# Performance work log

Measured on AMD Instinct MI355X. Metric: run time of the kernel, lower is better.

The kernel has to match this reference:

```python
import jax, jax.numpy as jnp
import numpy as np

# Fixed architecture constants (match init_kwargs)
B, CIN, H, W = 2, 3, 224, 224
COUT = 64
KH = KW = 7
SH = SW = 2
PAD = 3
GROUPS = 1
MIX = 4
CG = COUT // GROUPS          # channels per group
REL = CG // 2                # rel_size
PH, PW = H + 2 * PAD, W + 2 * PAD          # padded spatial dims (230, 230)
FH = (PH - KH) // SH + 1                    # output height (112)
FW = (PW - KW) // SW + 1                    # output width  (112)


def setup_inputs() -> dict:
    key = jax.random.key(0)
    ks = jax.random.split(key, 10)
    n = jax.random.normal
    return {
        "x": n(ks[0], (B, CIN, H, W), jnp.float32),
        "weight_query": n(ks[1], (GROUPS, CIN // GROUPS, CG), jnp.float32) * 0.2,
        "weight_key": n(ks[2], (GROUPS, CIN // GROUPS, CG), jnp.float32) * 0.2,
        "weight_value": n(ks[3], (MIX, GROUPS, CIN // GROUPS, CG), jnp.float32) * 0.2,
        "relative_x": n(ks[4], (REL, 1, KW), jnp.float32) * 0.1,
        "relative_y": n(ks[5], (CG - REL, KH, 1), jnp.float32) * 0.1,
        "emb_x": n(ks[6], (CG, 1, PW), jnp.float32) * 0.1,
        "emb_y": n(ks[7], (CG, PH, 1), jnp.float32) * 0.1,
        "emb_m": n(ks[8], (MIX, CG, 1, 1), jnp.float32) * 0.1,
        "bias": n(ks[9], (COUT,), jnp.float32) * 0.05,
    }


def _unfold(t):
    """torch.nn.functional.unfold: (b,c,PH,PW) -> (b,c,KH*KW,FH*FW) with (c,kh,kw) layout."""
    b, c = t.shape[0], t.shape[1]
    ri = jnp.arange(FH) * SH
    rj = jnp.arange(FW) * SW
    p = t[:, :, ri[:, None] + jnp.arange(KH)[None, :], :]          # (b,c,FH,KH,PW)
    p = p[:, :, :, :, rj[:, None] + jnp.arange(KW)[None, :]]       # (b,c,FH,KH,FW,KW)
    return p.transpose(0, 1, 3, 5, 2, 4).reshape(b, c, KH * KW, FH * FW)


def _forward(x, wq, wk, wv, rx, ry, ex, ey, em, bias):
    b = x.shape[0]
    # relative position bias: (COUT, KH*KW, 1)
    rel = jnp.concatenate([jnp.tile(rx, (1, KH, 1)), jnp.tile(ry, (1, 1, KW))], axis=0)
    rel = jnp.tile(rel, (GROUPS, 1, 1)).reshape(COUT, KH * KW, 1)

    xp = jnp.pad(x, ((0, 0), (0, 0), (PAD, PAD), (PAD, PAD)))       # (b,CIN,PH,PW)
    x_ij = xp.transpose(0, 2, 3, 1).reshape(b, PH * PW, GROUPS, CIN // GROUPS)

    # per-pixel grouped projections -> (b, COUT, PH, PW)
    vq = jnp.einsum('bngi,gio->bgon', x_ij, wq).reshape(b, COUT, PH, PW)
    vk = jnp.einsum('bngi,gio->bgon', x_ij, wk).reshape(b, COUT, PH, PW)

    # mixture weights over value transforms: softmax over mix axis, per pixel
    p_ab = ex + ey                                                   # (CG,PH,PW)
    p_abm = jax.nn.softmax(jnp.sum(p_ab[None] * em, axis=1), axis=0) # (MIX,PH,PW)

    vvm = jnp.einsum('bngi,mgio->mbgon', x_ij, wv).reshape(MIX, b, COUT, PH, PW)
    vv = jnp.sum(vvm * p_abm[:, None, None], axis=0)                 # (b,COUT,PH,PW)

    win_k = _unfold(vk)                                              # (b,COUT,KH*KW,L)
    win_v = _unfold(vv)                                              # (b,COUT,KH*KW,L)
    # center query of each window (equivalent to unfold then slice center)
    ci = (KH - 1) // 2 + jnp.arange(FH) * SH
    cj = (KW - 1) // 2 + jnp.arange(FW) * SW
    win_q = vq[:, :, ci[:, None], cj[None, :]].reshape(b, COUT, 1, FH * FW)

    scores = jnp.sum(win_q * (win_k + rel[None]), axis=1)            # (b,KH*KW,L)
    # NOTE: the torch code applies softmax over dim=2 which, after the sum over
    # channels, is the SPATIAL dim (L), not the window dim. Faithful to source.
    attn = jax.nn.softmax(scores, axis=2)                            # (b,KH*KW,L)
    v = jnp.sum(attn[:, None] * win_v, axis=2) + bias[None, :, None] # (b,COUT,L)
    return v.reshape(b, COUT, FH, FW)


def reference(x, weight_query, weight_key, weight_value, relative_x, relative_y, emb_x, emb_y, emb_m, bias):
    return _forward(x, weight_query, weight_key, weight_value, relative_x, relative_y, emb_x, emb_y, emb_m, bias)
```

## Files before the change

kernel.cpp:

```cpp
#include <hip/hip_runtime.h>
#include <math.h>

namespace {
constexpr int Bc = 2, Hc = 224, Wc = 224, HWc = Hc * Wc;
constexpr int COUTc = 64, KHc = 7, KWc = 7, PADc = 3;
constexpr int MIXc = 4, RELc = 32;
constexpr int PHc = 230, PWc = 230;
constexpr int FHc = 112, FWc = 112, NN = FHc * FWc;
constexpr int NK = KHc * KWc;
constexpr int NCHUNK = 196;
constexpr int WS_EEX = 0;
constexpr int WS_EEY = WS_EEX + MIXc * PWc;
constexpr int WS_COL = WS_EEY + MIXc * PHc;
constexpr int WS_PART = 1920;
}

__global__ __launch_bounds__(256) void sam_k0(
    const float* __restrict__ ex, const float* __restrict__ ey,
    const float* __restrict__ em, const float* __restrict__ wq,
    const float* __restrict__ wk, const float* __restrict__ rx,
    const float* __restrict__ ry, float* __restrict__ ws) {
  const int idx = blockIdx.x * 256 + threadIdx.x;
  constexpr int half = MIXc * PWc;
  if (idx < 2 * half) {
    const int which = idx >= half;
    const int r = which ? idx - half : idx;
    const int m = r / PWc, j = r % PWc;
    float s = 0.f;
#pragma unroll 8
    for (int c = 0; c < COUTc; ++c)
      s += (which ? ey[c * PHc + j] : ex[c * PWc + j]) * em[m * COUTc + c];
    ws[idx] = __expf(s);
  }
  const int u = idx - 2 * half;
  if (u >= 0 && u < 51) {
    float s = 0.f;
    if (u < 9) {
      const int cj = u / 3, ci = u % 3;
#pragma unroll 8
      for (int o = 0; o < COUTc; ++o) s += wq[cj * COUTc + o] * wk[ci * COUTc + o];
    } else if (u < 30) {
      const int v = u - 9, cj = v / 7, kw = v % 7;
#pragma unroll 8
      for (int o = 0; o < RELc; ++o) s += wq[cj * COUTc + o] * rx[o * KWc + kw];
    } else {
      const int v = u - 30, cj = v / 7, kh = v % 7;
#pragma unroll 8
      for (int o = 0; o < RELc; ++o) s += wq[cj * COUTc + RELc + o] * ry[o * KHc + kh];
    }
    ws[WS_COL + u] = s;
  }
}

__global__ __launch_bounds__(256) void sam_stats(const float* __restrict__ x,
                                                 float* __restrict__ ws) {
  __shared__ float sCol[51];
  const int t = threadIdx.x;
  if (t < 51) sCol[t] = ws[WS_COL + t];
  __syncthreads();

  const int w = t >> 6, lane = t & 63;
  const int k = blockIdx.y * 4 + w;
  if (k >= NK) return;
  const int b = blockIdx.z;
  const int kh = k / 7, kw = k - 7 * kh;
  const int n = blockIdx.x * 64 + lane;
  const int fh = n / FWc, fw = n - fh * FWc;
  const int i0 = 2 * fh, j0 = 2 * fw;
  const float* xb = x + (size_t)b * 3 * HWc;
  const int co = i0 * Wc + j0;
  const float xc0 = xb[co], xc1 = xb[HWc + co], xc2 = xb[2 * HWc + co];

  float s = xc0 * (sCol[9 + kw] + sCol[30 + kh]) +
            xc1 * (sCol[16 + kw] + sCol[37 + kh]) +
            xc2 * (sCol[23 + kw] + sCol[44 + kh]);
  const int ir = i0 + kh - PADc, jc = j0 + kw - PADc;
  if ((unsigned)ir < (unsigned)Hc && (unsigned)jc < (unsigned)Wc) {
    const float q0 = xc0 * sCol[0] + xc1 * sCol[3] + xc2 * sCol[6];
    const float q1 = xc0 * sCol[1] + xc1 * sCol[4] + xc2 * sCol[7];
    const float q2 = xc0 * sCol[2] + xc1 * sCol[5] + xc2 * sCol[8];
    const int off = ir * Wc + jc;
    s += q0 * xb[off] + q1 * xb[HWc + off] + q2 * xb[2 * HWc + off];
  }
  float e = __expf(s);
#pragma unroll
  for (int m2 = 32; m2; m2 >>= 1) e += __shfl_xor(e, m2, 64);
  if (lane == 0)
    ws[WS_PART + ((size_t)b * NK + k) * NCHUNK + blockIdx.x] = e;
}

__global__ __launch_bounds__(256) void sam_out(
    const float* __restrict__ x, const float* __restrict__ wv,
    const float* __restrict__ bias, const float* __restrict__ ws,
    float* __restrict__ out) {
  __shared__ float sCol[51];
  __shared__ float sdninv[NK];
  __shared__ float swv[12 * 64];
  __shared__ float sbias[64];
  __shared__ float sT[8][32][13];

  const int t = threadIdx.x;
  const int b = blockIdx.y;
  if (t < 51) sCol[t] = ws[WS_COL + t];
  if (t < 64) sbias[t] = bias[t];
  for (int i = t; i < 12 * 64; i += 256) swv[i] = wv[i];
  if (t < 4 * NK) {
    const int k = t >> 2, p = t & 3;
    const float* base = ws + WS_PART + ((size_t)b * NK + k) * NCHUNK;
    float s = 0.f;
    for (int c = p; c < NCHUNK; c += 4) s += base[c];
    s += __shfl_xor(s, 1, 64);
    s += __shfl_xor(s, 2, 64);
    if (p == 0) sdninv[k] = 1.f / s;
  }
  __syncthreads();

  const int g = t >> 5, px = t & 31;
  const int n = blockIdx.x * 32 + px;
  const int fh = n / FWc, fw = n - fh * FWc;
  const int i0 = 2 * fh, j0 = 2 * fw;
  const float* xb = x + (size_t)b * 3 * HWc;
  const int co = i0 * Wc + j0;
  const float xc0 = xb[co], xc1 = xb[HWc + co], xc2 = xb[2 * HWc + co];
  const float q0 = xc0 * sCol[0] + xc1 * sCol[3] + xc2 * sCol[6];
  const float q1 = xc0 * sCol[1] + xc1 * sCol[4] + xc2 * sCol[7];
  const float q2 = xc0 * sCol[2] + xc1 * sCol[5] + xc2 * sCol[8];

  const float* eEX = ws + WS_EEX;
  const float* eEY = ws + WS_EEY;

  float T[12] = {0.f};
#pragma unroll
  for (int it = 0; it < 7; ++it) {
    const int kk = g + 8 * it;
    if (kk < NK) {
      const int kh = kk / 7, kw = kk - 7 * ((kk * 9363) >> 16);
      const int kw2 = kk - 7 * kh;
      (void)kw;
      const int ir = i0 + kh - PADc, jc = j0 + kw2 - PADc;
      if ((unsigned)ir < (unsigned)Hc && (unsigned)jc < (unsigned)Wc) {
        float s = xc0 * (sCol[9 + kw2] + sCol[30 + kh]) +
                  xc1 * (sCol[16 + kw2] + sCol[37 + kh]) +
                  xc2 * (sCol[23 + kw2] + sCol[44 + kh]);
        const int off = ir * Wc + jc;
        const float x0 = xb[off], x1 = xb[HWc + off], x2 = xb[2 * HWc + off];
        s += q0 * x0 + q1 * x1 + q2 * x2;
        const float e = __expf(s) * sdninv[kk];
        const int ii = i0 + kh, jj = j0 + kw2;
        const float p0 = eEX[jj] * eEY[ii];
        const float p1 = eEX[PWc + jj] * eEY[PHc + ii];
        const float p2 = eEX[2 * PWc + jj] * eEY[2 * PHc + ii];
        const float p3 = eEX[3 * PWc + jj] * eEY[3 * PHc + ii];
        const float wgt = e * __builtin_amdgcn_rcpf(p0 + p1 + p2 + p3);
        const float a0 = wgt * p0, a1 = wgt * p1, a2 = wgt * p2, a3 = wgt * p3;
        T[0] += a0 * x0; T[1]  += a0 * x1; T[2]  += a0 * x2;
        T[3] += a1 * x0; T[4]  += a1 * x1; T[5]  += a1 * x2;
        T[6] += a2 * x0; T[7]  += a2 * x1; T[8]  += a2 * x2;
        T[9] += a3 * x0; T[10] += a3 * x1; T[11] += a3 * x2;
      }
    }
  }
#pragma unroll
  for (int j = 0; j < 12; ++j) sT[g][px][j] = T[j];
  __syncthreads();

  float Tm[12];
#pragma unroll
  for (int j = 0; j < 12; ++j) {
    float s = 0.f;
#pragma unroll
    for (int ww = 0; ww < 8; ++ww) s += sT[ww][px][j];
    Tm[j] = s;
  }
  float* ob = out + (size_t)b * COUTc * NN + n;
#pragma unroll
  for (int oo = 0; oo < 8; ++oo) {
    const int o = g * 8 + oo;
    float acc = sbias[o];
#pragma unroll
    for (int mc = 0; mc < 12; ++mc) acc += swv[mc * 64 + o] * Tm[mc];
    ob[(size_t)o * NN] = acc;
  }
}

extern "C" void kernel_launch(void* const* d_in, const int* in_sizes, int n_in,
                              void* d_out, int out_size, void* d_ws, size_t ws_size,
                              hipStream_t stream) {
  const float* x    = (const float*)d_in[0];
  const float* wq   = (const float*)d_in[1];
  const float* wk   = (const float*)d_in[2];
  const float* wv   = (const float*)d_in[3];
  const float* rx   = (const float*)d_in[4];
  const float* ry   = (const float*)d_in[5];
  const float* ex   = (const float*)d_in[6];
  const float* ey   = (const float*)d_in[7];
  const float* em   = (const float*)d_in[8];
  const float* bias = (const float*)d_in[9];
  float* out = (float*)d_out;
  float* ws  = (float*)d_ws;

  sam_k0<<<dim3(8), 256, 0, stream>>>(ex, ey, em, wq, wk, rx, ry, ws);
  sam_stats<<<dim3(NCHUNK, (NK + 3) / 4, Bc), 256, 0, stream>>>(x, ws);
  sam_out<<<dim3(NN / 32, Bc), 256, 0, stream>>>(x, wv, bias, ws, out);
}
```

Measured before the change: 107.4 us.

## Merge precompute into scores kernel, materialize exp scores, cache embeddings in LDS

Removes the separate tiny precompute kernel: every scores block recomputes the collapsed weight table, and the first eight blocks also build the exp embedding tables. The scores kernel now writes each exp score to a workspace array along with per-chunk partial sums, so the output kernel reads scores instead of recomputing them and keeps the embedding tables in shared memory. This drops one launch and duplicated exp work, at the cost of roughly 10 MB of extra global write/read traffic and redundant per-block weight collapses. It also seems to rely on the eight table-building blocks finishing before sam_out, which holds only because the kernels run in sequence.

```diff
diff --git a/kernel.cpp b/kernel.cpp
--- a/kernel.cpp
+++ b/kernel.cpp
@@ -3,120 +3,74 @@
 
 namespace {
 constexpr int Bc = 2, Hc = 224, Wc = 224, HWc = Hc * Wc;
-constexpr int COUTc = 64, KHc = 7, KWc = 7, PADc = 3;
+constexpr int COUTc = 64, PADc = 3;
 constexpr int MIXc = 4, RELc = 32;
 constexpr int PHc = 230, PWc = 230;
 constexpr int FHc = 112, FWc = 112, NN = FHc * FWc;
-constexpr int NK = KHc * KWc;
-constexpr int NCHUNK = 196;
+constexpr int NK = 49;
+constexpr int CH = 32;
+constexpr int NCH = NN / CH;
 constexpr int WS_EEX = 0;
 constexpr int WS_EEY = WS_EEX + MIXc * PWc;
-constexpr int WS_COL = WS_EEY + MIXc * PHc;
-constexpr int WS_PART = 1920;
-}
-
-__global__ __launch_bounds__(256) void sam_k0(
-    const float* __restrict__ ex, const float* __restrict__ ey,
-    const float* __restrict__ em, const float* __restrict__ wq,
+constexpr int WS_PART = WS_EEY + MIXc * PHc;
+constexpr int WS_E = WS_PART + Bc * NK * NCH;
+}
+
+__device__ __forceinline__ void collapse(const float* __restrict__ wq,
+                                         const float* __restrict__ wk,
+                                         const float* __restrict__ rx,
+                                         const float* __restrict__ ry,
+                                         float* sCol) {
+  const int t = threadIdx.x;
+  if (t < 51) {
+    float s = 0.f;
+    if (t < 9) {
+      const int cj = t / 3, ci = t % 3;
+#pragma unroll 8
+      for (int o = 0; o < COUTc; ++o) s += wq[cj * COUTc + o] * wk[ci * COUTc + o];
+    } else if (t < 30) {
+      const int v = t - 9, cj = v / 7, kw = v % 7;
+#pragma unroll 8
+      for (int o = 0; o < RELc; ++o) s += wq[cj * COUTc + o] * rx[o * 7 + kw];
+    } else {
+      const int v = t - 30, cj = v / 7, kh = v % 7;
+#pragma unroll 8
+      for (int o = 0; o < RELc; ++o) s += wq[cj * COUTc + RELc + o] * ry[o * 7 + kh];
+    }
+    sCol[t] = s;
+  }
+}
+
+__global__ __launch_bounds__(256) void sam_scores(
+    const float* __restrict__ x, const float* __restrict__ wq,
     const float* __restrict__ wk, const float* __restrict__ rx,
-    const float* __restrict__ ry, float* __restrict__ ws) {
-  const int idx = blockIdx.x * 256 + threadIdx.x;
-  constexpr int half = MIXc * PWc;
-  if (idx < 2 * half) {
-    const int which = idx >= half;
-    const int r = which ? idx - half : idx;
-    const int m = r / PWc, j = r % PWc;
-    float s = 0.f;
-#pragma unroll 8
-    for (int c = 0; c < COUTc; ++c)
-      s += (which ? ey[c * PHc + j] : ex[c * PWc + j]) * em[m * COUTc + c];
-    ws[idx] = __expf(s);
-  }
-  const int u = idx - 2 * half;
-  if (u >= 0 && u < 51) {
-    float s = 0.f;
-    if (u < 9) {
-      const int cj = u / 3, ci = u % 3;
-#pragma unroll 8
-      for (int o = 0; o < COUTc; ++o) s += wq[cj * COUTc + o] * wk[ci * COUTc + o];
-    } else if (u < 30) {
-      const int v = u - 9, cj = v / 7, kw = v % 7;
-#pragma unroll 8
-      for (int o = 0; o < RELc; ++o) s += wq[cj * COUTc + o] * rx[o * KWc + kw];
-    } else {
-      const int v = u - 30, cj = v / 7, kh = v % 7;
-#pragma unroll 8
-      for (int o = 0; o < RELc; ++o) s += wq[cj * COUTc + RELc + o] * ry[o * KHc + kh];
-    }
-    ws[WS_COL + u] = s;
-  }
-}
-
-__global__ __launch_bounds__(256) void sam_stats(const float* __restrict__ x,
-                                                 float* __restrict__ ws) {
+    const float* __restrict__ ry, const float* __restrict__ ex,
+    const float* __restrict__ ey, const float* __restrict__ em,
+    float* __restrict__ ws) {
   __shared__ float sCol[51];
   const int t = threadIdx.x;
-  if (t < 51) sCol[t] = ws[WS_COL + t];
+  const int c = blockIdx.x, b = blockIdx.y;
+  collapse(wq, wk, rx, ry, sCol);
+
+  const int bf = b * NCH + c;
+  if (bf < 8) {
+    const int idx = bf * 256 + t;
+    constexpr int half = MIXc * PWc;
+    if (idx < 2 * half) {
+      const int which = idx >= half;
+      const int r = which ? idx - half : idx;
+      const int m = r / PWc, j = r % PWc;
+      float s = 0.f;
+#pragma unroll 8
+      for (int cc = 0; cc < COUTc; ++cc)
+        s += (which ? ey[cc * PHc + j] : ex[cc * PWc + j]) * em[m * COUTc + cc];
+      ws[idx] = __expf(s);
+    }
+  }
   __syncthreads();
 
-  const int w = t >> 6, lane = t & 63;
-  const int k = blockIdx.y * 4 + w;
-  if (k >= NK) return;
-  const int b = blockIdx.z;
-  const int kh = k / 7, kw = k - 7 * kh;
-  const int n = blockIdx.x * 64 + lane;
-  const int fh = n / FWc, fw = n - fh * FWc;
-  const int i0 = 2 * fh, j0 = 2 * fw;
-  const float* xb = x + (size_t)b * 3 * HWc;
-  const int co = i0 * Wc + j0;
-  const float xc0 = xb[co], xc1 = xb[HWc + co], xc2 = xb[2 * HWc + co];
-
-  float s = xc0 * (sCol[9 + kw] + sCol[30 + kh]) +
-            xc1 * (sCol[16 + kw] + sCol[37 + kh]) +
-            xc2 * (sCol[23 + kw] + sCol[44 + kh]);
-  const int ir = i0 + kh - PADc, jc = j0 + kw - PADc;
-  if ((unsigned)ir < (unsigned)Hc && (unsigned)jc < (unsigned)Wc) {
-    const float q0 = xc0 * sCol[0] + xc1 * sCol[3] + xc2 * sCol[6];
-    const float q1 = xc0 * sCol[1] + xc1 * sCol[4] + xc2 * sCol[7];
-    const float q2 = xc0 * sCol[2] + xc1 * sCol[5] + xc2 * sCol[8];
-    const int off = ir * Wc + jc;
-    s += q0 * xb[off] + q1 * xb[HWc + off] + q2 * xb[2 * HWc + off];
-  }
-  float e = __expf(s);
-#pragma unroll
-  for (int m2 = 32; m2; m2 >>= 1) e += __shfl_xor(e, m2, 64);
-  if (lane == 0)
-    ws[WS_PART + ((size_t)b * NK + k) * NCHUNK + blockIdx.x] = e;
-}
-
-__global__ __launch_bounds__(256) void sam_out(
-    const float* __restrict__ x, const float* __restrict__ wv,
-    const float* __restrict__ bias, const float* __restrict__ ws,
-    float* __restrict__ out) {
-  __shared__ float sCol[51];
-  __shared__ float sdninv[NK];
-  __shared__ float swv[12 * 64];
-  __shared__ float sbias[64];
-  __shared__ float sT[8][32][13];
-
-  const int t = threadIdx.x;
-  const int b = blockIdx.y;
-  if (t < 51) sCol[t] = ws[WS_COL + t];
-  if (t < 64) sbias[t] = bias[t];
-  for (int i = t; i < 12 * 64; i += 256) swv[i] = wv[i];
-  if (t < 4 * NK) {
-    const int k = t >> 2, p = t & 3;
-    const float* base = ws + WS_PART + ((size_t)b * NK + k) * NCHUNK;
-    float s = 0.f;
-    for (int c = p; c < NCHUNK; c += 4) s += base[c];
-    s += __shfl_xor(s, 1, 64);
-    s += __shfl_xor(s, 2, 64);
-    if (p == 0) sdninv[k] = 1.f / s;
-  }
-  __syncthreads();
-
   const int g = t >> 5, px = t & 31;
-  const int n = blockIdx.x * 32 + px;
+  const int n = c * CH + px;
   const int fh = n / FWc, fw = n - fh * FWc;
   const int i0 = 2 * fh, j0 = 2 * fw;
   const float* xb = x + (size_t)b * 3 * HWc;
@@ -126,32 +80,86 @@
   const float q1 = xc0 * sCol[1] + xc1 * sCol[4] + xc2 * sCol[7];
   const float q2 = xc0 * sCol[2] + xc1 * sCol[5] + xc2 * sCol[8];
 
-  const float* eEX = ws + WS_EEX;
-  const float* eEY = ws + WS_EEY;
-
-  float T[12] = {0.f};
+  float* E = ws + WS_E;
+  float* part = ws + WS_PART;
 #pragma unroll
   for (int it = 0; it < 7; ++it) {
     const int kk = g + 8 * it;
     if (kk < NK) {
-      const int kh = kk / 7, kw = kk - 7 * ((kk * 9363) >> 16);
-      const int kw2 = kk - 7 * kh;
-      (void)kw;
-      const int ir = i0 + kh - PADc, jc = j0 + kw2 - PADc;
+      const int kh = kk / 7, kw = kk - 7 * kh;
+      float s = xc0 * (sCol[9 + kw] + sCol[30 + kh]) +
+                xc1 * (sCol[16 + kw] + sCol[37 + kh]) +
+                xc2 * (sCol[23 + kw] + sCol[44 + kh]);
+      const int ir = i0 + kh - PADc, jc = j0 + kw - PADc;
       if ((unsigned)ir < (unsigned)Hc && (unsigned)jc < (unsigned)Wc) {
-        float s = xc0 * (sCol[9 + kw2] + sCol[30 + kh]) +
-                  xc1 * (sCol[16 + kw2] + sCol[37 + kh]) +
-                  xc2 * (sCol[23 + kw2] + sCol[44 + kh]);
+        const int off = ir * Wc + jc;
+        s += q0 * xb[off] + q1 * xb[HWc + off] + q2 * xb[2 * HWc + off];
+      }
+      const float e = __expf(s);
+      E[(size_t)(b * NK + kk) * NN + n] = e;
+      float r = e;
+      r += __shfl_xor(r, 1, 64);
+      r += __shfl_xor(r, 2, 64);
+      r += __shfl_xor(r, 4, 64);
+      r += __shfl_xor(r, 8, 64);
+      r += __shfl_xor(r, 16, 64);
+      if (px == 0) part[(b * NK + kk) * NCH + c] = r;
+    }
+  }
+}
+
+__global__ __launch_bounds__(256) void sam_out(
+    const float* __restrict__ x, const float* __restrict__ wv,
+    const float* __restrict__ bias, const float* __restrict__ ws,
+    float* __restrict__ out) {
+  __shared__ float sEEX[MIXc * PWc];
+  __shared__ float sEEY[MIXc * PHc];
+  __shared__ float sdninv[NK];
+  __shared__ float swv[12 * 64];
+  __shared__ float sbias[64];
+  __shared__ float sT[8][32][13];
+
+  const int t = threadIdx.x;
+  const int c = blockIdx.x, b = blockIdx.y;
+  for (int i = t; i < MIXc * PWc; i += 256) sEEX[i] = ws[WS_EEX + i];
+  for (int i = t; i < MIXc * PHc; i += 256) sEEY[i] = ws[WS_EEY + i];
+  if (t < 64) sbias[t] = bias[t];
+  for (int i = t; i < 12 * 64; i += 256) swv[i] = wv[i];
+  if (t < 4 * NK) {
+    const int k = t >> 2, p = t & 3;
+    const float* base = ws + WS_PART + (b * NK + k) * NCH;
+    float s = 0.f;
+    for (int cc = p; cc < NCH; cc += 4) s += base[cc];
+    s += __shfl_xor(s, 1, 64);
+    s += __shfl_xor(s, 2, 64);
+    if (p == 0) sdninv[k] = 1.f / s;
+  }
+  __syncthreads();
+
+  const int g = t >> 5, px = t & 31;
+  const int n = c * CH + px;
+  const int fh = n / FWc, fw = n - fh * FWc;
+  const int i0 = 2 * fh, j0 = 2 * fw;
+  const float* xb = x + (size_t)b * 3 * HWc;
+  const float* E = ws + WS_E;
+
+  float T[12] = {0.f};
+#pragma unroll
+  for (int it = 0; it < 7; ++it) {
+    const int kk = g + 8 * it;
+    if (kk < NK) {
+      const int kh = kk / 7, kw = kk - 7 * kh;
+      const int ir = i0 + kh - PADc, jc = j0 + kw - PADc;
+      if ((unsigned)ir < (unsigned)Hc && (unsigned)jc < (unsigned)Wc) {
+        const float e = E[(size_t)(b * NK + kk) * NN + n] * sdninv[kk];
+        const int ii = i0 + kh, jj = j0 + kw;
+        const float p0 = sEEX[jj] * sEEY[ii];
+        const float p1 = sEEX[PWc + jj] * sEEY[PHc + ii];
+        const float p2 = sEEX[2 * PWc + jj] * sEEY[2 * PHc + ii];
+        const float p3 = sEEX[3 * PWc + jj] * sEEY[3 * PHc + ii];
+        const float wgt = e * __builtin_amdgcn_rcpf(p0 + p1 + p2 + p3);
         const int off = ir * Wc + jc;
         const float x0 = xb[off], x1 = xb[HWc + off], x2 = xb[2 * HWc + off];
-        s += q0 * x0 + q1 * x1 + q2 * x2;
-        const float e = __expf(s) * sdninv[kk];
-        const int ii = i0 + kh, jj = j0 + kw2;
-        const float p0 = eEX[jj] * eEY[ii];
-        const float p1 = eEX[PWc + jj] * eEY[PHc + ii];
-        const float p2 = eEX[2 * PWc + jj] * eEY[2 * PHc + ii];
-        const float p3 = eEX[3 * PWc + jj] * eEY[3 * PHc + ii];
-        const float wgt = e * __builtin_amdgcn_rcpf(p0 + p1 + p2 + p3);
         const float a0 = wgt * p0, a1 = wgt * p1, a2 = wgt * p2, a3 = wgt * p3;
         T[0] += a0 * x0; T[1]  += a0 * x1; T[2]  += a0 * x2;
         T[3] += a1 * x0; T[4]  += a1 * x1; T[5]  += a1 * x2;
@@ -199,7 +207,6 @@
   float* out = (float*)d_out;
   float* ws  = (float*)d_ws;
 
-  sam_k0<<<dim3(8), 256, 0, stream>>>(ex, ey, em, wq, wk, rx, ry, ws);
-  sam_stats<<<dim3(NCHUNK, (NK + 3) / 4, Bc), 256, 0, stream>>>(x, ws);
-  sam_out<<<dim3(NN / 32, Bc), 256, 0, stream>>>(x, wv, bias, ws, out);
-}
+  sam_scores<<<dim3(NCH, Bc), 256, 0, stream>>>(x, wq, wk, rx, ry, ex, ey, em, ws);
+  sam_out<<<dim3(NCH, Bc), 256, 0, stream>>>(x, wv, bias, ws, out);
+}
```

After: 113.2 us. 1.05x slower.
